# Performance work log

Hardware: AMD Instinct MI355X
Metric: run time of the kernel (lower is better)

The kernel has to match this reference:

```python
import jax, jax.numpy as jnp
import numpy as np

F, N, C, H, M = 256, 400, 128, 8, 128  # frames, batch*joints, mdl_channels, heads, max_pos
E = C // H


def _layer_norm(z, g, b, eps=1e-5):
    mu = jnp.mean(z, axis=-1, keepdims=True)
    var = jnp.mean((z - mu) ** 2, axis=-1, keepdims=True)
    return (z - mu) * jax.lax.rsqrt(var + eps) * g + b


def setup_inputs() -> dict:
    key = jax.random.key(0)
    ks = jax.random.split(key, 16)
    s = 0.02
    return {
        "x": jax.random.normal(ks[0], (F, N, C), jnp.float32),
        "tree_encoding": jax.random.normal(ks[1], (N, C), jnp.float32),
        "W_qkv": jax.random.normal(ks[2], (3 * C, C), jnp.float32) * s,      # Linear weight (out,in), no bias
        "W_tree_k": jax.random.normal(ks[3], (C, C), jnp.float32) * s,
        "W_tree_v": jax.random.normal(ks[4], (C, C), jnp.float32) * s,
        "emb": jax.random.normal(ks[5], (2 * M + 1, E), jnp.float32) * s,    # distance embedding table
        "W_beta": jax.random.normal(ks[6], (1, 3 * C), jnp.float32) * s,     # lin_beta (out,in), no bias
        "ln1_g": jnp.ones((C,), jnp.float32),
        "ln1_b": jnp.zeros((C,), jnp.float32),
        "ln2_g": jnp.ones((C,), jnp.float32),
        "ln2_b": jnp.zeros((C,), jnp.float32),
        "W1": jax.random.normal(ks[7], (C, C), jnp.float32) * s,
        "b1": jnp.zeros((C,), jnp.float32),
        "W2": jax.random.normal(ks[8], (C, C), jnp.float32) * s,
        "b2": jnp.zeros((C,), jnp.float32),
    }


def reference(x, tree_encoding, W_qkv, W_tree_k, W_tree_v, emb, W_beta,
              ln1_g, ln1_b, ln2_g, ln2_b, W1, b1, W2, b2):
    f, n, c = x.shape
    # qkv projection, no bias
    qkv = x @ W_qkv.T                          # (f, n, 3c)
    q, k, v = jnp.split(qkv, 3, axis=-1)       # each (f, n, c)
    # tree positional encoding added to key/value
    k = k + (tree_encoding @ W_tree_k)[None]
    v = v + (tree_encoding @ W_tree_v)[None]
    # (f, n, c) -> (n, f, h, e): n is the attention batch, f is sequence length
    to_heads = lambda t: t.transpose(1, 0, 2).reshape(n, f, H, E)
    qh, kh, vh = to_heads(q), to_heads(k), to_heads(v)
    # content scores
    qk = jnp.einsum('nlhe,nshe->nhls', qh, kh)
    # relative position bias
    ids = jnp.arange(f)
    dist = jnp.clip(ids[:, None] - ids[None, :], -M, M) + M   # (f, f)
    pe = emb[dist]                                            # (f, f, e)
    qk = qk + jnp.einsum('nlhe,lse->nhls', qh, pe)
    qk = qk + jnp.einsum('nshe,lse->nhls', kh, pe)
    scale = 1.0 / (E ** 0.5)
    att = jax.nn.softmax(qk * scale, axis=-1)                 # (n, h, f, f)
    out = jnp.einsum('nhls,nshe->nlhe', att, vh)              # (n, f, h, e)
    y = out.reshape(n, f, c).transpose(1, 0, 2)               # (f, n, c)
    # gated AddNorm (beta=True): x is residual, y is attention output
    gate = jax.nn.sigmoid(jnp.concatenate([y, x, y - x], axis=-1) @ W_beta.T)
    h1 = _layer_norm(gate * x + (1.0 - gate) * y, ln1_g, ln1_b)
    # FFN (GELU exact, as torch nn.GELU default)
    ff = jax.nn.gelu(h1 @ W1.T + b1, approximate=False) @ W2.T + b2
    return _layer_norm(ff + h1, ln2_g, ln2_b)
```

## Files before the change

kernel.cpp:

```cpp
#include <hip/hip_runtime.h>
#include <math.h>

#define F_DIM 256
#define N_DIM 400
#define C_DIM 128
#define H_DIM 8
#define E_DIM 16
#define ROWS  (F_DIM * N_DIM)
#define SBUF  (N_DIM * H_DIM * F_DIM * E_DIM)

#define S_SCALE 0.6005612043932249f

typedef _Float16 half2_t __attribute__((ext_vector_type(2)));
typedef _Float16 f16x8   __attribute__((ext_vector_type(8)));
typedef float    f32x16  __attribute__((ext_vector_type(16)));
typedef float    f32x4   __attribute__((ext_vector_type(4)));

struct H2x4 { half2_t h[4]; };

__device__ inline f16x8 pack8(float4 a, float4 b) {
    H2x4 t;
    t.h[0] = __builtin_bit_cast(half2_t, __builtin_amdgcn_cvt_pkrtz(a.x, a.y));
    t.h[1] = __builtin_bit_cast(half2_t, __builtin_amdgcn_cvt_pkrtz(a.z, a.w));
    t.h[2] = __builtin_bit_cast(half2_t, __builtin_amdgcn_cvt_pkrtz(b.x, b.y));
    t.h[3] = __builtin_bit_cast(half2_t, __builtin_amdgcn_cvt_pkrtz(b.z, b.w));
    return __builtin_bit_cast(f16x8, t);
}

__device__ inline _Float16 h_rtz(float v) {
    half2_t p = __builtin_bit_cast(half2_t, __builtin_amdgcn_cvt_pkrtz(v, v));
    return p[0];
}

__device__ inline int iclamp256(int v) { return v < 0 ? 0 : (v > 256 ? 256 : v); }

__global__ __launch_bounds__(256) void prep_pack(
    const float* __restrict__ x, const float* __restrict__ Wq,
    const float* __restrict__ emb, const float* __restrict__ te,
    const float* __restrict__ Wtk, const float* __restrict__ Wtv,
    _Float16* __restrict__ xh, _Float16* __restrict__ Wqh,
    _Float16* __restrict__ embh, float* __restrict__ tk, float* __restrict__ tv)
{
    int bid = blockIdx.x;
    int t   = threadIdx.x;
    if (bid < 6400) {
        int i = (bid * 256 + t) * 8;
        const float4* s = (const float4*)(x + i);
        *(uint4*)(xh + i) = __builtin_bit_cast(uint4, pack8(s[0], s[1]));
    } else if (bid < 6424) {
        int i = ((bid - 6400) * 256 + t) * 8;
        const float4* s = (const float4*)(Wq + i);
        *(uint4*)(Wqh + i) = __builtin_bit_cast(uint4, pack8(s[0], s[1]));
    } else if (bid < 6426) {
        int r = (bid - 6424) * 256 + t;
        if (r > 256) return;
        const float4* er = (const float4*)(emb + r * 16);
        float4 e0 = er[0], e1 = er[1], e2 = er[2], e3 = er[3];
        e0.x *= S_SCALE; e0.y *= S_SCALE; e0.z *= S_SCALE; e0.w *= S_SCALE;
        e1.x *= S_SCALE; e1.y *= S_SCALE; e1.z *= S_SCALE; e1.w *= S_SCALE;
        e2.x *= S_SCALE; e2.y *= S_SCALE; e2.z *= S_SCALE; e2.w *= S_SCALE;
        e3.x *= S_SCALE; e3.y *= S_SCALE; e3.z *= S_SCALE; e3.w *= S_SCALE;
        *(uint4*)(embh + r * 16)     = __builtin_bit_cast(uint4, pack8(e0, e1));
        *(uint4*)(embh + r * 16 + 8) = __builtin_bit_cast(uint4, pack8(e2, e3));
    } else {
        int n = bid - 6426;
        const float* W = (t < 128) ? Wtk : Wtv;
        float* outp    = (t < 128) ? tk : tv;
        int j = t & 127;
        float acc = 0.f;
        #pragma unroll 4
        for (int c = 0; c < 128; ++c)
            acc += te[n * 128 + c] * W[c * 128 + j];
        outp[n * 128 + j] = acc;
    }
}

__global__ __launch_bounds__(256) void qkv_gemm(
    const _Float16* __restrict__ xh, const _Float16* __restrict__ Wqh,
    const float* __restrict__ tk, const float* __restrict__ tv,
    _Float16* __restrict__ qn, _Float16* __restrict__ kn, _Float16* __restrict__ vn)
{
    int tid  = threadIdx.x;
    int wave = tid >> 6, lane = tid & 63;
    int m32  = lane & 31, khalf = lane >> 5;
    int row0 = blockIdx.y * 64 + (wave & 1) * 32;
    int col0 = blockIdx.x * 64 + (wave >> 1) * 32;

    const _Float16* xp = xh  + (row0 + m32) * 128 + khalf * 8;
    const _Float16* wp = Wqh + (col0 + m32) * 128 + khalf * 8;

    f32x16 acc;
    #pragma unroll
    for (int i = 0; i < 16; ++i) acc[i] = 0.f;

    #pragma unroll
    for (int k0 = 0; k0 < 128; k0 += 16) {
        f16x8 xa = __builtin_bit_cast(f16x8, *(const uint4*)(xp + k0));
        f16x8 wa = __builtin_bit_cast(f16x8, *(const uint4*)(wp + k0));
        acc = __builtin_amdgcn_mfma_f32_32x32x16_f16(xa, wa, acc, 0, 0, 0);
    }

    int o   = col0 + m32;
    int sec = o >> 7;
    int rem = o & 127;
    #pragma unroll
    for (int reg = 0; reg < 16; ++reg) {
        int r = row0 + (reg & 3) + 8 * (reg >> 2) + 4 * khalf;
        float val = acc[reg];
        if (sec == 0) {
            qn[r * 128 + rem] = h_rtz(val * S_SCALE);
        } else {
            int f = r / 400;
            int n = r - f * 400;
            if (sec == 1) {
                kn[r * 128 + rem] = h_rtz((val + tk[n * 128 + rem]) * S_SCALE);
            } else {
                vn[r * 128 + rem] = (_Float16)(val + tv[n * 128 + rem]);
            }
        }
    }
}

__global__ __launch_bounds__(256) void v_pack(
    const _Float16* __restrict__ vn, _Float16* __restrict__ vT)
{
    __shared__ _Float16 sm[16 * 264];
    int bn = blockIdx.x;
    int n  = bn >> 3, h = bn & 7;
    int t  = threadIdx.x;

    const uint4* src = (const uint4*)(vn + (t * 400 + n) * 128 + h * 16);
    uint4 a = src[0], b = src[1];
    union { uint4 u; _Float16 hv[8]; } ua, ub;
    ua.u = a; ub.u = b;
    #pragma unroll
    for (int e = 0; e < 8; ++e) sm[e * 264 + t]       = ua.hv[e];
    #pragma unroll
    for (int e = 0; e < 8; ++e) sm[(e + 8) * 264 + t] = ub.hv[e];
    __syncthreads();

    #pragma unroll
    for (int k = 0; k < 2; ++k) {
        int idx = (k * 256 + t) * 8;
        int e = idx >> 8, f0 = idx & 255;
        uint4 o = *(const uint4*)(sm + e * 264 + f0);
        *(uint4*)(vT + bn * 4096 + idx) = o;
    }
}

#define R2_STRIDE 258
#define PS_STRIDE 40

__global__ __launch_bounds__(256, 4) void attn_kernel(
    const _Float16* __restrict__ qb, const _Float16* __restrict__ kb,
    const _Float16* __restrict__ vb, const _Float16* __restrict__ embh,
    _Float16* __restrict__ y)
{
    __shared__ __align__(16) _Float16 R2sh[32 * R2_STRIDE];
    __shared__ __align__(16) _Float16 Psh[4 * 32 * PS_STRIDE];

    int tid  = threadIdx.x;
    int wave = tid >> 6, lane = tid & 63;
    int bid  = blockIdx.x;
    int bn   = (bid & 7) * 400 + (bid >> 3);
    int n    = bn >> 3, h = bn & 7;
    int base = bn * 4096;

    int nn  = lane & 31;
    int kh  = lane >> 5;
    int khb = (lane & 32) << 2;
    int cbase = 31 + 4 * kh - nn;
    int dbase = 4 * kh - nn;
    int q16 = (lane >> 4) & 3;

    int nat_off = n * 128 + h * 16 + kh * 8;

    f16x8 aq[2];
    #pragma unroll
    for (int lt = 0; lt < 2; ++lt)
        aq[lt] = __builtin_bit_cast(f16x8,
            *(const uint4*)(qb + (64 * wave + 32 * lt + nn) * 51200 + nat_off));

    f16x8 bones;
    #pragma unroll
    for (int i = 0; i < 8; ++i) bones[i] = (_Float16)1.0f;

    f32x4 O[2][2];
    f32x4 Od[2][2];
    #pragma unroll
    for (int i = 0; i < 2; ++i)
        #pragma unroll
        for (int j = 0; j < 2; ++j)
            #pragma unroll
            for (int r = 0; r < 4; ++r) { O[i][j][r] = 0.f; Od[i][j][r] = 0.f; }

    _Float16* psw = Psh + wave * 32 * PS_STRIDE;

    for (int st = 0; st < 8; ++st) {
        f16x8 bk = __builtin_bit_cast(f16x8,
            *(const uint4*)(kb + (32 * st + nn) * 51200 + nat_off));

        for (int ct = wave; ct < 9; ct += 4) {
            int erow = 32 * ct + nn; if (erow > 256) erow = 256;
            f16x8 be = __builtin_bit_cast(f16x8,
                *(const uint4*)(embh + erow * 16 + kh * 8));
            f32x16 c2;
            #pragma unroll
            for (int i = 0; i < 16; ++i) c2[i] = 0.f;
            c2 = __builtin_amdgcn_mfma_f32_32x32x16_f16(bk, be, c2, 0, 0, 0);
            int col = 32 * ct + nn;
            if (col <= 257) {
                #pragma unroll
                for (int r = 0; r < 16; ++r) {
                    int srow = (r & 3) + 8 * (r >> 2) + 4 * kh;
                    R2sh[srow * R2_STRIDE + col] = (_Float16)c2[r];
                }
            }
        }
        __syncthreads();

        f16x8 bv = __builtin_bit_cast(f16x8,
            *(const uint4*)(vb + base + (lane & 15) * 256 + 32 * st + q16 * 8));

        #pragma unroll
        for (int lt = 0; lt < 2; ++lt) {
            int U0 = 64 * wave + 32 * lt - 32 * st + 128;

            f32x16 S;
            #pragma unroll
            for (int i = 0; i < 16; ++i) S[i] = 0.f;
            S = __builtin_amdgcn_mfma_f32_32x32x16_f16(aq[lt], bk, S, 0, 0, 0);

            int br0 = iclamp256(U0 - 31 + nn);
            int br1 = iclamp256(U0 + 1 + nn);
            f16x8 be0 = __builtin_bit_cast(f16x8,
                *(const uint4*)(embh + br0 * 16 + kh * 8));
            f16x8 be1 = __builtin_bit_cast(f16x8,
                *(const uint4*)(embh + br1 * 16 + kh * 8));
            f32x16 W0, W1;
            #pragma unroll
            for (int i = 0; i < 16; ++i) { W0[i] = 0.f; W1[i] = 0.f; }
            W0 = __builtin_amdgcn_mfma_f32_32x32x16_f16(aq[lt], be0, W0, 0, 0, 0);
            W1 = __builtin_amdgcn_mfma_f32_32x32x16_f16(aq[lt], be1, W1, 0, 0, 0);

            #pragma unroll
            for (int r = 0; r < 16; ++r) {
                int rmr = (r & 3) + 8 * (r >> 2);
                int c   = rmr + cbase;
                int addr = ((c & 31) << 2) + khb;
                int w01 = __builtin_bit_cast(int,
                    __builtin_amdgcn_cvt_pkrtz(W0[r], W1[r]));
                half2_t hh = __builtin_bit_cast(half2_t,
                    __builtin_amdgcn_ds_bpermute(addr, w01));
                float b1 = (float)((c < 32) ? hh[0] : hh[1]);
                int d = iclamp256(U0 + rmr + dbase);
                float b2 = (float)R2sh[nn * R2_STRIDE + d];
                float p = exp2f(S[r] + b1 + b2);
                int mloc = rmr + 4 * kh;
                psw[mloc * PS_STRIDE + nn] = (_Float16)p;
            }

            #pragma unroll
            for (int a = 0; a < 2; ++a) {
                f16x8 ap = __builtin_bit_cast(f16x8,
                    *(const uint4*)(psw + (16 * a + (lane & 15)) * PS_STRIDE + q16 * 8));
                O[lt][a]  = __builtin_amdgcn_mfma_f32_16x16x32_f16(ap, bv,    O[lt][a],  0, 0, 0);
                Od[lt][a] = __builtin_amdgcn_mfma_f32_16x16x32_f16(ap, bones, Od[lt][a], 0, 0, 0);
            }
        }
        __syncthreads();
    }

    #pragma unroll
    for (int lt = 0; lt < 2; ++lt) {
        #pragma unroll
        for (int a = 0; a < 2; ++a) {
            #pragma unroll
            for (int r = 0; r < 4; ++r) {
                int row  = q16 * 4 + r;
                int lloc = 32 * lt + 16 * a + row;
                int lg = 64 * wave + lloc;
                y[(lg * 400 + n) * 128 + h * 16 + (lane & 15)] =
                    (_Float16)(O[lt][a][r] / Od[lt][a][r]);
            }
        }
    }
}

__global__ __launch_bounds__(256) void gate_ln1(
    const float* __restrict__ x, const _Float16* __restrict__ yh,
    const float* __restrict__ Wb, const float* __restrict__ g,
    const float* __restrict__ b, float* __restrict__ h1)
{
    int tid  = threadIdx.x;
    int r    = blockIdx.x * 4 + (tid >> 6);
    int lane = tid & 63;
    int c    = lane * 2;

    float2 xv = *(const float2*)(x + r * 128 + c);
    half2_t yv2 = *(const half2_t*)(yh + r * 128 + c);
    float yvx = (float)yv2[0], yvy = (float)yv2[1];
    float2 w0 = *(const float2*)(Wb + c);
    float2 w1 = *(const float2*)(Wb + 128 + c);
    float2 w2 = *(const float2*)(Wb + 256 + c);

    float sv = yvx * w0.x + yvy * w0.y
             + xv.x * w1.x + xv.y * w1.y
             + (yvx - xv.x) * w2.x + (yvy - xv.y) * w2.y;
    #pragma unroll
    for (int off = 32; off > 0; off >>= 1) sv += __shfl_xor(sv, off);
    float gate = 1.0f / (1.0f + __expf(-sv));

    float z0 = gate * xv.x + (1.0f - gate) * yvx;
    float z1 = gate * xv.y + (1.0f - gate) * yvy;
    float s1 = z0 + z1, s2 = z0 * z0 + z1 * z1;
    #pragma unroll
    for (int off = 32; off > 0; off >>= 1) {
        s1 += __shfl_xor(s1, off);
        s2 += __shfl_xor(s2, off);
    }
    float mu  = s1 * (1.0f / 128.0f);
    float var = s2 * (1.0f / 128.0f) - mu * mu;
    float rs  = rsqrtf(var + 1e-5f);

    float2 gv = *(const float2*)(g + c);
    float2 bv = *(const float2*)(b + c);
    float2 ov;
    ov.x = (z0 - mu) * rs * gv.x + bv.x;
    ov.y = (z1 - mu) * rs * gv.y + bv.y;
    *(float2*)(h1 + r * 128 + c) = ov;
}

__global__ __launch_bounds__(256) void ff1_gemm(
    const float* __restrict__ A, const float* __restrict__ W,
    const float* __restrict__ bias, _Float16* __restrict__ outp)
{
    int tid  = threadIdx.x;
    int wave = tid >> 6, lane = tid & 63;
    int m32  = lane & 31, khalf = lane >> 5;
    int row0 = blockIdx.y * 64 + (wave & 1) * 32;
    int col0 = blockIdx.x * 64 + (wave >> 1) * 32;

    const float* ap = A + (row0 + m32) * 128 + khalf * 8;
    const float* wp = W + (col0 + m32) * 128 + khalf * 8;

    f32x16 acc;
    #pragma unroll
    for (int i = 0; i < 16; ++i) acc[i] = 0.f;

    #pragma unroll
    for (int k0 = 0; k0 < 128; k0 += 16) {
        float4 aa = *(const float4*)(ap + k0);
        float4 ab = *(const float4*)(ap + k0 + 4);
        float4 wa = *(const float4*)(wp + k0);
        float4 wb = *(const float4*)(wp + k0 + 4);
        acc = __builtin_amdgcn_mfma_f32_32x32x16_f16(pack8(aa, ab), pack8(wa, wb), acc, 0, 0, 0);
    }

    int   c  = col0 + m32;
    float bi = bias[c];
    #pragma unroll
    for (int reg = 0; reg < 16; ++reg) {
        int r = row0 + (reg & 3) + 8 * (reg >> 2) + 4 * khalf;
        float v = acc[reg] + bi;
        v = 0.5f * v * (1.0f + erff(v * 0.70710678118654752f));
        outp[r * 128 + c] = (_Float16)v;
    }
}

__global__ __launch_bounds__(256) void ff2_ln2(
    const _Float16* __restrict__ A, const float* __restrict__ W2,
    const float* __restrict__ b2, const float* __restrict__ h1,
    const float* __restrict__ g, const float* __restrict__ bb,
    float* __restrict__ outp)
{
    __shared__ float Cs[32 * 132];
    int tid  = threadIdx.x;
    int wave = tid >> 6, lane = tid & 63;
    int m32  = lane & 31, khalf = lane >> 5;
    int row0 = blockIdx.x * 32;
    int col0 = wave * 32;

    const _Float16* ap = A  + (row0 + m32) * 128 + khalf * 8;
    const float*    wp = W2 + (col0 + m32) * 128 + khalf * 8;

    f32x16 acc;
    #pragma unroll
    for (int i = 0; i < 16; ++i) acc[i] = 0.f;

    #pragma unroll
    for (int k0 = 0; k0 < 128; k0 += 16) {
        f16x8 aa16 = __builtin_bit_cast(f16x8, *(const uint4*)(ap + k0));
        float4 wa = *(const float4*)(wp + k0);
        float4 wb = *(const float4*)(wp + k0 + 4);
        acc = __builtin_amdgcn_mfma_f32_32x32x16_f16(aa16, pack8(wa, wb), acc, 0, 0, 0);
    }

    #pragma unroll
    for (int reg = 0; reg < 16; ++reg) {
        int rloc = (reg & 3) + 8 * (reg >> 2) + 4 * khalf;
        Cs[rloc * 132 + col0 + m32] = acc[reg];
    }
    __syncthreads();

    int rloc = tid >> 3, seg = (tid & 7) * 16;
    int r = row0 + rloc;
    float z[16];
    float s1 = 0.f, s2 = 0.f;
    #pragma unroll
    for (int j4 = 0; j4 < 4; ++j4) {
        float4 cv = *(const float4*)(Cs + rloc * 132 + seg + j4 * 4);
        float4 hv = *(const float4*)(h1 + r * 128 + seg + j4 * 4);
        float4 bv = *(const float4*)(b2 + seg + j4 * 4);
        z[j4*4+0] = cv.x + bv.x + hv.x;
        z[j4*4+1] = cv.y + bv.y + hv.y;
        z[j4*4+2] = cv.z + bv.z + hv.z;
        z[j4*4+3] = cv.w + bv.w + hv.w;
        s1 += z[j4*4+0] + z[j4*4+1] + z[j4*4+2] + z[j4*4+3];
        s2 += z[j4*4+0]*z[j4*4+0] + z[j4*4+1]*z[j4*4+1]
            + z[j4*4+2]*z[j4*4+2] + z[j4*4+3]*z[j4*4+3];
    }
    #pragma unroll
    for (int off = 4; off > 0; off >>= 1) {
        s1 += __shfl_xor(s1, off);
        s2 += __shfl_xor(s2, off);
    }
    float mu  = s1 * (1.0f / 128.0f);
    float var = s2 * (1.0f / 128.0f) - mu * mu;
    float rs  = rsqrtf(var + 1e-5f);
    #pragma unroll
    for (int j4 = 0; j4 < 4; ++j4) {
        float4 gv = *(const float4*)(g  + seg + j4 * 4);
        float4 bv = *(const float4*)(bb + seg + j4 * 4);
        float4 ov;
        ov.x = (z[j4*4+0] - mu) * rs * gv.x + bv.x;
        ov.y = (z[j4*4+1] - mu) * rs * gv.y + bv.y;
        ov.z = (z[j4*4+2] - mu) * rs * gv.z + bv.z;
        ov.w = (z[j4*4+3] - mu) * rs * gv.w + bv.w;
        *(float4*)(outp + r * 128 + seg + j4 * 4) = ov;
    }
}

extern "C" void kernel_launch(void* const* d_in, const int* in_sizes, int n_in,
                              void* d_out, int out_size, void* d_ws, size_t ws_size,
                              hipStream_t stream)
{
    const float* x     = (const float*)d_in[0];
    const float* te    = (const float*)d_in[1];
    const float* Wqkv  = (const float*)d_in[2];
    const float* Wtk   = (const float*)d_in[3];
    const float* Wtv   = (const float*)d_in[4];
    const float* emb   = (const float*)d_in[5];
    const float* Wbeta = (const float*)d_in[6];
    const float* ln1g  = (const float*)d_in[7];
    const float* ln1b  = (const float*)d_in[8];
    const float* ln2g  = (const float*)d_in[9];
    const float* ln2b  = (const float*)d_in[10];
    const float* W1    = (const float*)d_in[11];
    const float* b1    = (const float*)d_in[12];
    const float* W2    = (const float*)d_in[13];
    const float* b2    = (const float*)d_in[14];
    float* outp = (float*)d_out;

    float* ws = (float*)d_ws;
    float* tk = ws;
    float* tv = ws + 51200;
    float* qb_region = ws + 102400;
    float* kb_region = qb_region + SBUF;
    float* vb_region = kb_region + SBUF;
    float* yb        = vb_region + SBUF;

    _Float16* qnat = (_Float16*)qb_region;
    _Float16* knat = (_Float16*)kb_region;
    _Float16* vnat = (_Float16*)vb_region;
    _Float16* vT   = (_Float16*)(vb_region + SBUF / 2);
    _Float16* embh = (_Float16*)(qb_region + SBUF / 2);
    _Float16* yh   = (_Float16*)yb;
    _Float16* xh   = (_Float16*)(kb_region + SBUF / 2);
    _Float16* Wqh  = (_Float16*)(yb + SBUF / 2);

    float*    h1   = kb_region;
    _Float16* ff1h = (_Float16*)qb_region;

    prep_pack<<<6826, 256, 0, stream>>>(x, Wqkv, emb, te, Wtk, Wtv,
                                        xh, Wqh, embh, tk, tv);
    qkv_gemm<<<dim3(6, 1600), 256, 0, stream>>>(xh, Wqh, tk, tv, qnat, knat, vnat);
    v_pack<<<3200, 256, 0, stream>>>(vnat, vT);
    attn_kernel<<<3200, 256, 0, stream>>>(qnat, knat, vT, embh, yh);
    gate_ln1<<<ROWS / 4, 256, 0, stream>>>(x, yh, Wbeta, ln1g, ln1b, h1);
    ff1_gemm<<<dim3(2, 1600), 256, 0, stream>>>(h1, W1, b1, ff1h);
    ff2_ln2<<<3200, 256, 0, stream>>>(ff1h, W2, b2, h1, ln2g, ln2b, outp);
}
```

Before: 531.3 us.

## Split attention block across eight waves, one 32-row query tile each

```diff
diff --git a/kernel.cpp b/kernel.cpp
--- a/kernel.cpp
+++ b/kernel.cpp
@@ -151,13 +151,13 @@
 #define R2_STRIDE 258
 #define PS_STRIDE 40
 
-__global__ __launch_bounds__(256, 4) void attn_kernel(
+__global__ __launch_bounds__(512, 4) void attn_kernel(
     const _Float16* __restrict__ qb, const _Float16* __restrict__ kb,
     const _Float16* __restrict__ vb, const _Float16* __restrict__ embh,
     _Float16* __restrict__ y)
 {
     __shared__ __align__(16) _Float16 R2sh[32 * R2_STRIDE];
-    __shared__ __align__(16) _Float16 Psh[4 * 32 * PS_STRIDE];
+    __shared__ __align__(16) _Float16 Psh[8 * 32 * PS_STRIDE];
 
     int tid  = threadIdx.x;
     int wave = tid >> 6, lane = tid & 63;
@@ -175,24 +175,19 @@
 
     int nat_off = n * 128 + h * 16 + kh * 8;
 
-    f16x8 aq[2];
-    #pragma unroll
-    for (int lt = 0; lt < 2; ++lt)
-        aq[lt] = __builtin_bit_cast(f16x8,
-            *(const uint4*)(qb + (64 * wave + 32 * lt + nn) * 51200 + nat_off));
+    f16x8 aq = __builtin_bit_cast(f16x8,
+        *(const uint4*)(qb + (32 * wave + nn) * 51200 + nat_off));
 
     f16x8 bones;
     #pragma unroll
     for (int i = 0; i < 8; ++i) bones[i] = (_Float16)1.0f;
 
-    f32x4 O[2][2];
-    f32x4 Od[2][2];
-    #pragma unroll
-    for (int i = 0; i < 2; ++i)
-        #pragma unroll
-        for (int j = 0; j < 2; ++j)
-            #pragma unroll
-            for (int r = 0; r < 4; ++r) { O[i][j][r] = 0.f; Od[i][j][r] = 0.f; }
+    f32x4 O[2];
+    f32x4 Od[2];
+    #pragma unroll
+    for (int a = 0; a < 2; ++a)
+        #pragma unroll
+        for (int r = 0; r < 4; ++r) { O[a][r] = 0.f; Od[a][r] = 0.f; }
 
     _Float16* psw = Psh + wave * 32 * PS_STRIDE;
 
@@ -200,7 +195,7 @@
         f16x8 bk = __builtin_bit_cast(f16x8,
             *(const uint4*)(kb + (32 * st + nn) * 51200 + nat_off));
 
-        for (int ct = wave; ct < 9; ct += 4) {
+        for (int ct = wave; ct < 9; ct += 8) {
             int erow = 32 * ct + nn; if (erow > 256) erow = 256;
             f16x8 be = __builtin_bit_cast(f16x8,
                 *(const uint4*)(embh + erow * 16 + kh * 8));
@@ -222,67 +217,68 @@
         f16x8 bv = __builtin_bit_cast(f16x8,
             *(const uint4*)(vb + base + (lane & 15) * 256 + 32 * st + q16 * 8));
 
-        #pragma unroll
-        for (int lt = 0; lt < 2; ++lt) {
-            int U0 = 64 * wave + 32 * lt - 32 * st + 128;
-
-            f32x16 S;
-            #pragma unroll
-            for (int i = 0; i < 16; ++i) S[i] = 0.f;
-            S = __builtin_amdgcn_mfma_f32_32x32x16_f16(aq[lt], bk, S, 0, 0, 0);
-
-            int br0 = iclamp256(U0 - 31 + nn);
-            int br1 = iclamp256(U0 + 1 + nn);
-            f16x8 be0 = __builtin_bit_cast(f16x8,
-                *(const uint4*)(embh + br0 * 16 + kh * 8));
-            f16x8 be1 = __builtin_bit_cast(f16x8,
-                *(const uint4*)(embh + br1 * 16 + kh * 8));
-            f32x16 W0, W1;
-            #pragma unroll
-            for (int i = 0; i < 16; ++i) { W0[i] = 0.f; W1[i] = 0.f; }
-            W0 = __builtin_amdgcn_mfma_f32_32x32x16_f16(aq[lt], be0, W0, 0, 0, 0);
-            W1 = __builtin_amdgcn_mfma_f32_32x32x16_f16(aq[lt], be1, W1, 0, 0, 0);
-
-            #pragma unroll
-            for (int r = 0; r < 16; ++r) {
-                int rmr = (r & 3) + 8 * (r >> 2);
-                int c   = rmr + cbase;
-                int addr = ((c & 31) << 2) + khb;
-                int w01 = __builtin_bit_cast(int,
-                    __builtin_amdgcn_cvt_pkrtz(W0[r], W1[r]));
-                half2_t hh = __builtin_bit_cast(half2_t,
-                    __builtin_amdgcn_ds_bpermute(addr, w01));
-                float b1 = (float)((c < 32) ? hh[0] : hh[1]);
-                int d = iclamp256(U0 + rmr + dbase);
-                float b2 = (float)R2sh[nn * R2_STRIDE + d];
-                float p = exp2f(S[r] + b1 + b2);
-                int mloc = rmr + 4 * kh;
-                psw[mloc * PS_STRIDE + nn] = (_Float16)p;
-            }
-
-            #pragma unroll
-            for (int a = 0; a < 2; ++a) {
-                f16x8 ap = __builtin_bit_cast(f16x8,
-                    *(const uint4*)(psw + (16 * a + (lane & 15)) * PS_STRIDE + q16 * 8));
-                O[lt][a]  = __builtin_amdgcn_mfma_f32_16x16x32_f16(ap, bv,    O[lt][a],  0, 0, 0);
-                Od[lt][a] = __builtin_amdgcn_mfma_f32_16x16x32_f16(ap, bones, Od[lt][a], 0, 0, 0);
-            }
+        int U0 = 32 * wave - 32 * st + 128;
+
+        f32x16 S;
+        #pragma unroll
+        for (int i = 0; i < 16; ++i) S[i] = 0.f;
+        S = __builtin_amdgcn_mfma_f32_32x32x16_f16(aq, bk, S, 0, 0, 0);
+
+        int br0 = iclamp256(U0 - 31 + nn);
+        int br1 = iclamp256(U0 + 1 + nn);
+        f16x8 be0 = __builtin_bit_cast(f16x8,
+            *(const uint4*)(embh + br0 * 16 + kh * 8));
+        f16x8 be1 = __builtin_bit_cast(f16x8,
+            *(const uint4*)(embh + br1 * 16 + kh * 8));
+        f32x16 W0, W1;
+        #pragma unroll
+        for (int i = 0; i < 16; ++i) { W0[i] = 0.f; W1[i] = 0.f; }
+        W0 = __builtin_amdgcn_mfma_f32_32x32x16_f16(aq, be0, W0, 0, 0, 0);
+        W1 = __builtin_amdgcn_mfma_f32_32x32x16_f16(aq, be1, W1, 0, 0, 0);
+
+        half2_t b1p[8];
+        #pragma unroll
+        for (int r = 0; r < 16; ++r) {
+            int rmr = (r & 3) + 8 * (r >> 2);
+            int c   = rmr + cbase;
+            int addr = ((c & 31) << 2) + khb;
+            int w01 = __builtin_bit_cast(int,
+                __builtin_amdgcn_cvt_pkrtz(W0[r], W1[r]));
+            half2_t hh = __builtin_bit_cast(half2_t,
+                __builtin_amdgcn_ds_bpermute(addr, w01));
+            b1p[r >> 1][r & 1] = (c < 32) ? hh[0] : hh[1];
+        }
+
+        #pragma unroll
+        for (int r = 0; r < 16; ++r) {
+            int rmr = (r & 3) + 8 * (r >> 2);
+            float b1 = (float)b1p[r >> 1][r & 1];
+            int d = iclamp256(U0 + rmr + dbase);
+            float b2 = (float)R2sh[nn * R2_STRIDE + d];
+            float p = __builtin_amdgcn_exp2f(S[r] + b1 + b2);
+            int mloc = rmr + 4 * kh;
+            psw[mloc * PS_STRIDE + nn] = (_Float16)p;
+        }
+
+        #pragma unroll
+        for (int a = 0; a < 2; ++a) {
+            f16x8 ap = __builtin_bit_cast(f16x8,
+                *(const uint4*)(psw + (16 * a + (lane & 15)) * PS_STRIDE + q16 * 8));
+            O[a]  = __builtin_amdgcn_mfma_f32_16x16x32_f16(ap, bv,    O[a],  0, 0, 0);
+            Od[a] = __builtin_amdgcn_mfma_f32_16x16x32_f16(ap, bones, Od[a], 0, 0, 0);
         }
         __syncthreads();
     }
 
     #pragma unroll
-    for (int lt = 0; lt < 2; ++lt) {
-        #pragma unroll
-        for (int a = 0; a < 2; ++a) {
-            #pragma unroll
-            for (int r = 0; r < 4; ++r) {
-                int row  = q16 * 4 + r;
-                int lloc = 32 * lt + 16 * a + row;
-                int lg = 64 * wave + lloc;
-                y[(lg * 400 + n) * 128 + h * 16 + (lane & 15)] =
-                    (_Float16)(O[lt][a][r] / Od[lt][a][r]);
-            }
+    for (int a = 0; a < 2; ++a) {
+        #pragma unroll
+        for (int r = 0; r < 4; ++r) {
+            int row  = q16 * 4 + r;
+            int lloc = 16 * a + row;
+            int lg = 32 * wave + lloc;
+            y[(lg * 400 + n) * 128 + h * 16 + (lane & 15)] =
+                (_Float16)(O[a][r] / Od[a][r]);
         }
     }
 }
@@ -486,7 +482,7 @@
                                         xh, Wqh, embh, tk, tv);
     qkv_gemm<<<dim3(6, 1600), 256, 0, stream>>>(xh, Wqh, tk, tv, qnat, knat, vnat);
     v_pack<<<3200, 256, 0, stream>>>(vnat, vT);
-    attn_kernel<<<3200, 256, 0, stream>>>(qnat, knat, vT, embh, yh);
+    attn_kernel<<<3200, 512, 0, stream>>>(qnat, knat, vT, embh, yh);
     gate_ln1<<<ROWS / 4, 256, 0, stream>>>(x, yh, Wbeta, ln1g, ln1b, h1);
     ff1_gemm<<<dim3(2, 1600), 256, 0, stream>>>(h1, W1, b1, ff1h);
     ff2_ln2<<<3200, 256, 0, stream>>>(ff1h, W2, b2, h1, ln2g, ln2b, outp);
```

Result: no change. 525.8 us (-1.0%).
